# Kernel optimization log

Measured on AMD Instinct MI355X. Metric: run time of the kernel, lower is better.

The kernel has to match this reference:

```python
import jax, jax.numpy as jnp
import numpy as np

D = 128        # feature dim (hard-coded 128 split in source)
C = 16         # number of classes
N_S = 1600     # support set size (C * 100 shots)
Q = 32768      # number of query samples
HID = 128      # Class_Adap hidden width


def _class_centers(support_feat_inv, support_features, support_labels):
    # per-class mean of both support tensors (ComputeClassCenters)
    ones = jnp.ones((support_labels.shape[0],), support_feat_inv.dtype)
    counts = jax.ops.segment_sum(ones, support_labels, num_segments=C)
    counts = jnp.maximum(counts, 1.0)[:, None]                     # [C,1]
    mean_s = jax.ops.segment_sum(support_feat_inv, support_labels, num_segments=C) / counts   # [C,D]
    pre_s = jax.ops.segment_sum(support_features, support_labels, num_segments=C) / counts    # [C,D]
    return mean_s, pre_s


def setup_inputs() -> dict:
    key = jax.random.key(0)
    ks = jax.random.split(key, 6)
    return {
        "support_feat_inv": jax.random.normal(ks[0], (N_S, D), jnp.float32),
        "support_features": jax.random.normal(ks[1], (N_S, D), jnp.float32),
        "query_features": jax.random.normal(ks[2], (Q, D), jnp.float32),
        "W1": jax.random.normal(ks[3], (2 * D + 1, HID), jnp.float32) * 0.05,
        "b1": jnp.zeros((HID,), jnp.float32),
        "W2": jax.random.normal(ks[4], (HID, 1), jnp.float32) * 0.05,
        "b2": jnp.zeros((1,), jnp.float32),
        "support_labels": jax.random.randint(ks[5], (N_S,), 0, C),
        "query_labels": jax.random.randint(jax.random.fold_in(key, 7), (Q,), 0, C),
    }


def reference(support_feat_inv, support_features, query_features, W1, b1, W2, b2,
              support_labels, query_labels) -> jnp.ndarray:
    mean_s, pre_s = _class_centers(support_feat_inv, support_features, support_labels)
    q = query_features[:, None, :]                                  # [Q,1,D]
    gated = jax.nn.sigmoid(mean_s)[None, :, :] * q                  # [Q,C,D]
    q_full = jnp.broadcast_to(q, gated.shape)                       # [Q,C,D]
    inp = jnp.concatenate([q_full, gated], axis=-1)                 # [Q,C,2D]
    # AdaptiveAvgPool2d((None, D)) on [C,1,2D]: average adjacent pairs along last dim
    pooled = inp.reshape(Q, C, D, 2).mean(axis=-1)                  # [Q,C,D]
    # inner/outer product: sum(pre_support * query) per class
    outer = jnp.sum(pre_s[None, :, :] * q, axis=-1, keepdims=True)  # [Q,C,1]
    ext = jnp.concatenate([inp, outer], axis=-1)                    # [Q,C,2D+1]
    # Class_Adap tiny MLP -> per-class scalar weight
    h = jax.nn.relu(jnp.einsum('qce,eh->qch', ext, W1) + b1)        # [Q,C,HID]
    w = jax.nn.sigmoid(jnp.einsum('qch,ho->qco', h, W2) + b2)       # [Q,C,1]
    agg = jnp.sum(pooled * w, axis=1)                               # [Q,D]
    return agg + query_features                                     # residual (query_feature[0])
```

## Files before the change

### kernel.cpp

```cpp
#include <hip/hip_runtime.h>
#include <hip/hip_bf16.h>
#include <stdint.h>

#define DD 128
#define CC 16
#define NS 1600
#define QQ 32768
#define NBLK 64

typedef __attribute__((ext_vector_type(8))) short short8;
typedef __attribute__((ext_vector_type(4))) float f32x4;

__device__ inline short f2bf(float x) {
  union { float f; uint32_t u; } v; v.f = x;
  uint32_t r = (v.u + 0x7FFFu + ((v.u >> 16) & 1u)) >> 16;
  return (short)r;
}

__device__ inline uint32_t pk2bf(float lo, float hi) {
  __hip_bfloat162 h = __float22bfloat162_rn(make_float2(lo, hi));
  union { __hip_bfloat162 h2; uint32_t u; } v; v.h2 = h;
  return v.u;
}

__global__ __launch_bounds__(256) void centers_partial(
    const float* __restrict__ sfi, const float* __restrict__ sf,
    const int* __restrict__ labels, float* __restrict__ partA,
    float* __restrict__ partB, float* __restrict__ pcnt) {
  __shared__ float accA[2][CC][DD];
  __shared__ float accB[2][CC][DD];
  __shared__ float cnt[2][CC];
  const int t = threadIdx.x;
  const int d = t & 127, s = t >> 7;
  for (int i = t; i < 2 * CC * DD; i += 256) {
    ((float*)accA)[i] = 0.f;
    ((float*)accB)[i] = 0.f;
  }
  if (t < 2 * CC) ((float*)cnt)[t] = 0.f;
  __syncthreads();

  const int base = blockIdx.x * (NS / NBLK);
  for (int i = s; i < NS / NBLK; i += 2) {
    const int r = base + i;
    const int lbl = labels[r];
    accA[s][lbl][d] += sfi[(size_t)r * DD + d];
    accB[s][lbl][d] += sf[(size_t)r * DD + d];
    if (d == 0) cnt[s][lbl] += 1.f;
  }
  __syncthreads();

  float* pa = partA + (size_t)blockIdx.x * (CC * DD);
  float* pb = partB + (size_t)blockIdx.x * (CC * DD);
  for (int i = t; i < CC * DD; i += 256) {
    pa[i] = ((float*)accA)[i] + ((float*)accA)[CC * DD + i];
    pb[i] = ((float*)accB)[i] + ((float*)accB)[CC * DD + i];
  }
  if (t < CC) pcnt[blockIdx.x * CC + t] = cnt[0][t] + cnt[1][t];
}

__global__ __launch_bounds__(256) void build_wt_kernel(
    const float* __restrict__ W1, const float* __restrict__ partA,
    const float* __restrict__ partB, const float* __restrict__ pcnt,
    float* __restrict__ sg_out, short* __restrict__ WtTg) {
  __shared__ float sgc[DD], prc[DD];
  const int c = blockIdx.x, t = threadIdx.x;

  float cnt = 0.f;
  for (int b = 0; b < NBLK; ++b) cnt += pcnt[b * CC + c];
  cnt = fmaxf(cnt, 1.f);
  if (t < 128) {
    float a = 0.f;
    for (int b = 0; b < NBLK; ++b) a += partA[(size_t)b * (CC * DD) + c * DD + t];
    const float m = a / cnt;
    const float s = 1.f / (1.f + expf(-m));
    sgc[t] = s;
    sg_out[c * DD + t] = s;
  } else {
    const int d = t - 128;
    float a = 0.f;
    for (int b = 0; b < NBLK; ++b) a += partB[(size_t)b * (CC * DD) + c * DD + d];
    prc[d] = a / cnt;
  }
  __syncthreads();

  for (int it = 0; it < 8; ++it) {
    const int u = it * 256 + t;
    const int w_ = u >> 8;
    const int kb = (u >> 6) & 3;
    const int lane = u & 63;
    const int j = w_ * 16 + (lane & 15);
    const int e0 = kb * 32 + (lane >> 4) * 8;
    short8 r;
#pragma unroll
    for (int rr = 0; rr < 8; ++rr) {
      const int e = e0 + rr;
      float v = W1[e * DD + j] + sgc[e] * W1[(DD + e) * DD + j] +
                prc[e] * W1[2 * DD * DD + j];
      r[rr] = f2bf(v);
    }
    *(short8*)(WtTg + ((size_t)c * 2048 + u) * 8) = r;
  }
}

__global__ __launch_bounds__(512, 2) void main_kernel(
    const float* __restrict__ qf, const short* __restrict__ WtTg,
    const float* __restrict__ b1, const float* __restrict__ W2,
    const float* __restrict__ b2, float* __restrict__ w_ws) {
  __shared__ float p_part[8][CC][128];

  const int tid = threadIdx.x;
  const int lane = tid & 63;
  const int w = tid >> 6;
  const int l15 = lane & 15, l4 = lane >> 4;
  const int qbase = blockIdx.x * 128;

  short8 bq[8][4];
#pragma unroll
  for (int qn = 0; qn < 8; ++qn) {
    const float* qrow = qf + (size_t)(qbase + qn * 16 + l15) * DD;
#pragma unroll
    for (int kb = 0; kb < 4; ++kb) {
      const float* p0 = qrow + kb * 32 + l4 * 8;
      f32x4 f0 = *(const f32x4*)(p0);
      f32x4 f1 = *(const f32x4*)(p0 + 4);
      union { short8 s; uint32_t u[4]; } r;
      r.u[0] = pk2bf(f0[0], f0[1]);
      r.u[1] = pk2bf(f0[2], f0[3]);
      r.u[2] = pk2bf(f1[0], f1[1]);
      r.u[3] = pk2bf(f1[2], f1[3]);
      bq[qn][kb] = r.s;
    }
  }

  const f32x4 b1v = *(const f32x4*)(b1 + w * 16 + l4 * 4);
  const f32x4 w2v = *(const f32x4*)(W2 + w * 16 + l4 * 4);
  const float b2s = b2[0];

  const char* wbase = (const char*)WtTg + w * 4096 + lane * 16;

#define LOADW(dst, cls)                                                     \
  {                                                                         \
    _Pragma("unroll") for (int kb = 0; kb < 4; ++kb) dst[kb] =              \
        *(const short8*)(wbase + (size_t)(cls)*32768 + kb * 1024);          \
  }

#define COMPUTE(wf, cls)                                                    \
  {                                                                         \
    f32x4 acc[8];                                                           \
    _Pragma("unroll") for (int qn = 0; qn < 8; ++qn) acc[qn] = b1v;         \
    _Pragma("unroll") for (int kb = 0; kb < 4; ++kb)                        \
        _Pragma("unroll") for (int qn = 0; qn < 8; ++qn) acc[qn] =          \
            __builtin_amdgcn_mfma_f32_16x16x32_bf16(wf[kb], bq[qn][kb],     \
                                                    acc[qn], 0, 0, 0);      \
    _Pragma("unroll") for (int qn = 0; qn < 8; ++qn) {                      \
      float p = 0.f;                                                        \
      _Pragma("unroll") for (int i = 0; i < 4; ++i)                         \
          p += fmaxf(acc[qn][i], 0.f) * w2v[i];                             \
      p += __shfl_xor(p, 16);                                               \
      p += __shfl_xor(p, 32);                                               \
      if (l4 == 0) p_part[w][cls][qn * 16 + l15] = p;                       \
    }                                                                       \
  }

  short8 wfA[4], wfB[4];
  LOADW(wfA, 0);
  for (int c = 0; c < CC; c += 2) {
    LOADW(wfB, c + 1);
    COMPUTE(wfA, c);
    if (c + 2 < CC) LOADW(wfA, c + 2);
    COMPUTE(wfB, c + 1);
  }
#undef LOADW
#undef COMPUTE

  __syncthreads();

  {
    const int q = tid & 127;
    const int cg = tid >> 7;
    float pv[4];
#pragma unroll
    for (int k = 0; k < 4; ++k) {
      const int c = cg * 4 + k;
      float s = 0.f;
#pragma unroll
      for (int wv = 0; wv < 8; ++wv) s += p_part[wv][c][q];
      pv[k] = 1.f / (1.f + __expf(-(s + b2s)));
    }
    f32x4 o = {pv[0], pv[1], pv[2], pv[3]};
    *(f32x4*)(w_ws + ((size_t)(qbase + q)) * 16 + cg * 4) = o;
  }
}

__global__ __launch_bounds__(256) void agg_kernel(
    const float* __restrict__ qf, const float* __restrict__ sg,
    const float* __restrict__ w_ws, float* __restrict__ out) {
  const int t = threadIdx.x;
  const int s = t >> 5;
  const int ec = t & 31;
  const int e0 = ec * 4;
  const int qbase = blockIdx.x * 64;

  float4 sgv[16];
#pragma unroll
  for (int c = 0; c < 16; ++c) sgv[c] = *(const float4*)(sg + c * DD + e0);

  for (int qi = 0; qi < 8; ++qi) {
    const int q = qbase + qi * 8 + s;
    const float* wr = w_ws + (size_t)q * 16;
    float4 w0 = *(const float4*)(wr);
    float4 w1 = *(const float4*)(wr + 4);
    float4 w2 = *(const float4*)(wr + 8);
    float4 w3 = *(const float4*)(wr + 12);
    const float wc[16] = {w0.x, w0.y, w0.z, w0.w, w1.x, w1.y, w1.z, w1.w,
                          w2.x, w2.y, w2.z, w2.w, w3.x, w3.y, w3.z, w3.w};
    float Sv = 0.f;
#pragma unroll
    for (int c = 0; c < 16; ++c) Sv += wc[c];

    f32x4 sgw = {0.f, 0.f, 0.f, 0.f};
#pragma unroll
    for (int c = 0; c < 16; ++c) {
      sgw.x += wc[c] * sgv[c].x;
      sgw.y += wc[c] * sgv[c].y;
      sgw.z += wc[c] * sgv[c].z;
      sgw.w += wc[c] * sgv[c].w;
    }

    const float* qrow = qf + (size_t)q * DD;
    float4 qa = *(const float4*)(qrow + e0);
    float2 qd = *(const float2*)(qrow + 2 * ec);
    float2 qu = *(const float2*)(qrow + 64 + 2 * ec);

    float2 lo, hi;
    lo.x = 0.5f * (qa.x + qa.y) * Sv + qd.x;
    lo.y = 0.5f * (qa.z + qa.w) * Sv + qd.y;
    hi.x = 0.5f * (qa.x * sgw.x + qa.y * sgw.y) + qu.x;
    hi.y = 0.5f * (qa.z * sgw.z + qa.w * sgw.w) + qu.y;

    float* orow = out + (size_t)q * DD;
    *(float2*)(orow + 2 * ec) = lo;
    *(float2*)(orow + 64 + 2 * ec) = hi;
  }
}

extern "C" void kernel_launch(void* const* d_in, const int* in_sizes, int n_in,
                              void* d_out, int out_size, void* d_ws, size_t ws_size,
                              hipStream_t stream) {
  const float* sfi = (const float*)d_in[0];
  const float* sf  = (const float*)d_in[1];
  const float* qf  = (const float*)d_in[2];
  const float* W1  = (const float*)d_in[3];
  const float* b1  = (const float*)d_in[4];
  const float* W2  = (const float*)d_in[5];
  const float* b2  = (const float*)d_in[6];
  const int* slab  = (const int*)d_in[7];
  float* out = (float*)d_out;

  float* sg    = (float*)d_ws;
  float* w_ws  = sg + CC * DD;
  short* WtTg  = (short*)(w_ws + (size_t)QQ * CC);
  float* partA = (float*)(WtTg + CC * DD * DD);
  float* partB = partA + NBLK * CC * DD;
  float* pcnt  = partB + NBLK * CC * DD;

  centers_partial<<<NBLK, 256, 0, stream>>>(sfi, sf, slab, partA, partB, pcnt);
  build_wt_kernel<<<CC, 256, 0, stream>>>(W1, partA, partB, pcnt, sg, WtTg);
  main_kernel<<<QQ / 128, 512, 0, stream>>>(qf, WtTg, b1, W2, b2, w_ws);
  agg_kernel<<<QQ / 64, 256, 0, stream>>>(qf, sg, w_ws, out);
}
```

Before: 65.92 us.

## Pre-convert queries to bf16 in prep kernel and halve main kernel tile

Result: faster. 57.22 us (-13.2%).

```diff
diff --git a/kernel.cpp b/kernel.cpp
--- a/kernel.cpp
+++ b/kernel.cpp
@@ -9,6 +9,7 @@
 #define NBLK 64
 
 typedef __attribute__((ext_vector_type(8))) short short8;
+typedef __attribute__((ext_vector_type(4))) short short4v;
 typedef __attribute__((ext_vector_type(4))) float f32x4;
 
 __device__ inline short f2bf(float x) {
@@ -23,14 +24,30 @@
   return v.u;
 }
 
-__global__ __launch_bounds__(256) void centers_partial(
+__global__ __launch_bounds__(256) void prep_kernel(
     const float* __restrict__ sfi, const float* __restrict__ sf,
-    const int* __restrict__ labels, float* __restrict__ partA,
-    float* __restrict__ partB, float* __restrict__ pcnt) {
+    const int* __restrict__ labels, const float* __restrict__ qf,
+    float* __restrict__ partA, float* __restrict__ partB,
+    float* __restrict__ pcnt, short* __restrict__ qbf) {
+  const int t = threadIdx.x;
+
+  if (blockIdx.x >= NBLK) {
+    const size_t cb = (size_t)(blockIdx.x - NBLK) * (128 * DD);
+#pragma unroll
+    for (int i = 0; i < 16; ++i) {
+      const size_t off = cb + ((size_t)i * 256 + t) * 4;
+      f32x4 f = *(const f32x4*)(qf + off);
+      union { short4v s; uint32_t u[2]; } r;
+      r.u[0] = pk2bf(f[0], f[1]);
+      r.u[1] = pk2bf(f[2], f[3]);
+      *(short4v*)(qbf + off) = r.s;
+    }
+    return;
+  }
+
   __shared__ float accA[2][CC][DD];
   __shared__ float accB[2][CC][DD];
   __shared__ float cnt[2][CC];
-  const int t = threadIdx.x;
   const int d = t & 127, s = t >> 7;
   for (int i = t; i < 2 * CC * DD; i += 256) {
     ((float*)accA)[i] = 0.f;
@@ -102,34 +119,25 @@
   }
 }
 
-__global__ __launch_bounds__(512, 2) void main_kernel(
-    const float* __restrict__ qf, const short* __restrict__ WtTg,
+__global__ __launch_bounds__(512, 4) void main_kernel(
+    const short* __restrict__ qbf, const short* __restrict__ WtTg,
     const float* __restrict__ b1, const float* __restrict__ W2,
     const float* __restrict__ b2, float* __restrict__ w_ws) {
-  __shared__ float p_part[8][CC][128];
+  __shared__ float p_part[8][CC][64];
 
   const int tid = threadIdx.x;
   const int lane = tid & 63;
   const int w = tid >> 6;
   const int l15 = lane & 15, l4 = lane >> 4;
-  const int qbase = blockIdx.x * 128;
-
-  short8 bq[8][4];
-#pragma unroll
-  for (int qn = 0; qn < 8; ++qn) {
-    const float* qrow = qf + (size_t)(qbase + qn * 16 + l15) * DD;
-#pragma unroll
-    for (int kb = 0; kb < 4; ++kb) {
-      const float* p0 = qrow + kb * 32 + l4 * 8;
-      f32x4 f0 = *(const f32x4*)(p0);
-      f32x4 f1 = *(const f32x4*)(p0 + 4);
-      union { short8 s; uint32_t u[4]; } r;
-      r.u[0] = pk2bf(f0[0], f0[1]);
-      r.u[1] = pk2bf(f0[2], f0[3]);
-      r.u[2] = pk2bf(f1[0], f1[1]);
-      r.u[3] = pk2bf(f1[2], f1[3]);
-      bq[qn][kb] = r.s;
-    }
+  const int qbase = blockIdx.x * 64;
+
+  short8 bq[4][4];
+#pragma unroll
+  for (int qn = 0; qn < 4; ++qn) {
+    const short* qrow = qbf + (size_t)(qbase + qn * 16 + l15) * DD;
+#pragma unroll
+    for (int kb = 0; kb < 4; ++kb)
+      bq[qn][kb] = *(const short8*)(qrow + kb * 32 + l4 * 8);
   }
 
   const f32x4 b1v = *(const f32x4*)(b1 + w * 16 + l4 * 4);
@@ -146,19 +154,29 @@
 
 #define COMPUTE(wf, cls)                                                    \
   {                                                                         \
-    f32x4 acc[8];                                                           \
-    _Pragma("unroll") for (int qn = 0; qn < 8; ++qn) acc[qn] = b1v;         \
-    _Pragma("unroll") for (int kb = 0; kb < 4; ++kb)                        \
-        _Pragma("unroll") for (int qn = 0; qn < 8; ++qn) acc[qn] =          \
-            __builtin_amdgcn_mfma_f32_16x16x32_bf16(wf[kb], bq[qn][kb],     \
-                                                    acc[qn], 0, 0, 0);      \
-    _Pragma("unroll") for (int qn = 0; qn < 8; ++qn) {                      \
-      float p = 0.f;                                                        \
-      _Pragma("unroll") for (int i = 0; i < 4; ++i)                         \
-          p += fmaxf(acc[qn][i], 0.f) * w2v[i];                             \
-      p += __shfl_xor(p, 16);                                               \
-      p += __shfl_xor(p, 32);                                               \
-      if (l4 == 0) p_part[w][cls][qn * 16 + l15] = p;                       \
+    _Pragma("unroll") for (int qp = 0; qp < 2; ++qp) {                      \
+      f32x4 a0 = b1v, a1 = b1v;                                             \
+      _Pragma("unroll") for (int kb = 0; kb < 4; ++kb) {                    \
+        a0 = __builtin_amdgcn_mfma_f32_16x16x32_bf16(wf[kb],                \
+                                                     bq[2 * qp][kb], a0,    \
+                                                     0, 0, 0);              \
+        a1 = __builtin_amdgcn_mfma_f32_16x16x32_bf16(wf[kb],                \
+                                                     bq[2 * qp + 1][kb],    \
+                                                     a1, 0, 0, 0);          \
+      }                                                                     \
+      float p0 = 0.f, p1 = 0.f;                                             \
+      _Pragma("unroll") for (int i = 0; i < 4; ++i) {                       \
+        p0 += fmaxf(a0[i], 0.f) * w2v[i];                                   \
+        p1 += fmaxf(a1[i], 0.f) * w2v[i];                                   \
+      }                                                                     \
+      p0 += __shfl_xor(p0, 16);                                             \
+      p0 += __shfl_xor(p0, 32);                                             \
+      p1 += __shfl_xor(p1, 16);                                             \
+      p1 += __shfl_xor(p1, 32);                                             \
+      if (l4 == 0) {                                                        \
+        p_part[w][cls][(2 * qp) * 16 + l15] = p0;                           \
+        p_part[w][cls][(2 * qp + 1) * 16 + l15] = p1;                       \
+      }                                                                     \
     }                                                                       \
   }
 
@@ -176,19 +194,18 @@
   __syncthreads();
 
   {
-    const int q = tid & 127;
-    const int cg = tid >> 7;
-    float pv[4];
-#pragma unroll
-    for (int k = 0; k < 4; ++k) {
-      const int c = cg * 4 + k;
-      float s = 0.f;
-#pragma unroll
-      for (int wv = 0; wv < 8; ++wv) s += p_part[wv][c][q];
-      pv[k] = 1.f / (1.f + __expf(-(s + b2s)));
-    }
-    f32x4 o = {pv[0], pv[1], pv[2], pv[3]};
-    *(f32x4*)(w_ws + ((size_t)(qbase + q)) * 16 + cg * 4) = o;
+    const int q = tid & 63;
+    const int cg = tid >> 6;
+    float s0 = 0.f, s1 = 0.f;
+#pragma unroll
+    for (int wv = 0; wv < 8; ++wv) {
+      s0 += p_part[wv][cg * 2][q];
+      s1 += p_part[wv][cg * 2 + 1][q];
+    }
+    float2 o;
+    o.x = 1.f / (1.f + __expf(-(s0 + b2s)));
+    o.y = 1.f / (1.f + __expf(-(s1 + b2s)));
+    *(float2*)(w_ws + ((size_t)(qbase + q)) * 16 + cg * 2) = o;
   }
 }
 
@@ -263,9 +280,11 @@
   float* partA = (float*)(WtTg + CC * DD * DD);
   float* partB = partA + NBLK * CC * DD;
   float* pcnt  = partB + NBLK * CC * DD;
-
-  centers_partial<<<NBLK, 256, 0, stream>>>(sfi, sf, slab, partA, partB, pcnt);
+  short* qbf   = (short*)(pcnt + NBLK * CC);
+
+  prep_kernel<<<NBLK + QQ / 128, 256, 0, stream>>>(sfi, sf, slab, qf, partA,
+                                                   partB, pcnt, qbf);
   build_wt_kernel<<<CC, 256, 0, stream>>>(W1, partA, partB, pcnt, sg, WtTg);
-  main_kernel<<<QQ / 128, 512, 0, stream>>>(qf, WtTg, b1, W2, b2, w_ws);
+  main_kernel<<<QQ / 64, 512, 0, stream>>>(qbf, WtTg, b1, W2, b2, w_ws);
   agg_kernel<<<QQ / 64, 256, 0, stream>>>(qf, sg, w_ws, out);
 }
```

## Fuse aggregation into MLP kernel and halve queries per block

Applied to the files above, without the earlier changes.

Result: slower. 85.01 us (+28.9%).

```diff
diff --git a/kernel.cpp b/kernel.cpp
--- a/kernel.cpp
+++ b/kernel.cpp
@@ -102,21 +102,23 @@
   }
 }
 
-__global__ __launch_bounds__(512, 2) void main_kernel(
+__global__ __launch_bounds__(512, 4) void main_kernel(
     const float* __restrict__ qf, const short* __restrict__ WtTg,
     const float* __restrict__ b1, const float* __restrict__ W2,
-    const float* __restrict__ b2, float* __restrict__ w_ws) {
-  __shared__ float p_part[8][CC][128];
+    const float* __restrict__ b2, const float* __restrict__ sg,
+    float* __restrict__ out) {
+  __shared__ __align__(16) char p_lds[65536];
+  __shared__ float w_lds[64][17];
 
   const int tid = threadIdx.x;
   const int lane = tid & 63;
   const int w = tid >> 6;
   const int l15 = lane & 15, l4 = lane >> 4;
-  const int qbase = blockIdx.x * 128;
-
-  short8 bq[8][4];
-#pragma unroll
-  for (int qn = 0; qn < 8; ++qn) {
+  const int qbase = blockIdx.x * 64;
+
+  short8 bq[4][4];
+#pragma unroll
+  for (int qn = 0; qn < 4; ++qn) {
     const float* qrow = qf + (size_t)(qbase + qn * 16 + l15) * DD;
 #pragma unroll
     for (int kb = 0; kb < 4; ++kb) {
@@ -146,101 +148,98 @@
 
 #define COMPUTE(wf, cls)                                                    \
   {                                                                         \
-    f32x4 acc[8];                                                           \
-    _Pragma("unroll") for (int qn = 0; qn < 8; ++qn) acc[qn] = b1v;         \
-    _Pragma("unroll") for (int kb = 0; kb < 4; ++kb)                        \
-        _Pragma("unroll") for (int qn = 0; qn < 8; ++qn) acc[qn] =          \
-            __builtin_amdgcn_mfma_f32_16x16x32_bf16(wf[kb], bq[qn][kb],     \
-                                                    acc[qn], 0, 0, 0);      \
-    _Pragma("unroll") for (int qn = 0; qn < 8; ++qn) {                      \
-      float p = 0.f;                                                        \
-      _Pragma("unroll") for (int i = 0; i < 4; ++i)                         \
-          p += fmaxf(acc[qn][i], 0.f) * w2v[i];                             \
-      p += __shfl_xor(p, 16);                                               \
-      p += __shfl_xor(p, 32);                                               \
-      if (l4 == 0) p_part[w][cls][qn * 16 + l15] = p;                       \
+    f32x4 pv;                                                               \
+    _Pragma("unroll") for (int qp = 0; qp < 2; ++qp) {                      \
+      f32x4 a0 = b1v, a1 = b1v;                                             \
+      _Pragma("unroll") for (int kb = 0; kb < 4; ++kb) {                    \
+        a0 = __builtin_amdgcn_mfma_f32_16x16x32_bf16(wf[kb],                \
+                                                     bq[2 * qp][kb], a0,    \
+                                                     0, 0, 0);              \
+        a1 = __builtin_amdgcn_mfma_f32_16x16x32_bf16(wf[kb],                \
+                                                     bq[2 * qp + 1][kb],    \
+                                                     a1, 0, 0, 0);          \
+      }                                                                     \
+      float p0 = 0.f, p1 = 0.f;                                             \
+      _Pragma("unroll") for (int i = 0; i < 4; ++i) {                       \
+        p0 += fmaxf(a0[i], 0.f) * w2v[i];                                   \
+        p1 += fmaxf(a1[i], 0.f) * w2v[i];                                   \
+      }                                                                     \
+      pv[2 * qp] = p0;                                                      \
+      pv[2 * qp + 1] = p1;                                                  \
     }                                                                       \
+    *(f32x4*)(p_lds + (((cls)&7) * 8 + w) * 1024 + lane * 16) = pv;         \
+  }
+
+#define REDUCE(hf)                                                          \
+  {                                                                         \
+    __syncthreads();                                                        \
+    if (tid < 128) {                                                        \
+      const int c7 = tid >> 4, lr = tid & 15;                               \
+      f32x4 vacc = {0.f, 0.f, 0.f, 0.f};                                    \
+      _Pragma("unroll") for (int wv = 0; wv < 8; ++wv)                      \
+          _Pragma("unroll") for (int g = 0; g < 4; ++g) vacc +=             \
+          *(const f32x4*)(p_lds + (c7 * 8 + wv) * 1024 + (g * 16 + lr) * 16);\
+      _Pragma("unroll") for (int qn = 0; qn < 4; ++qn)                      \
+          w_lds[qn * 16 + lr][(hf)*8 + c7] =                                \
+              1.f / (1.f + __expf(-(vacc[qn] + b2s)));                      \
+    }                                                                       \
+    __syncthreads();                                                        \
   }
 
   short8 wfA[4], wfB[4];
   LOADW(wfA, 0);
-  for (int c = 0; c < CC; c += 2) {
-    LOADW(wfB, c + 1);
-    COMPUTE(wfA, c);
-    if (c + 2 < CC) LOADW(wfA, c + 2);
-    COMPUTE(wfB, c + 1);
+#pragma unroll
+  for (int cp = 0; cp < CC; cp += 2) {
+    LOADW(wfB, cp + 1);
+    COMPUTE(wfA, cp);
+    if (cp + 2 < CC) LOADW(wfA, cp + 2);
+    COMPUTE(wfB, cp + 1);
+    if (cp == 6) REDUCE(0);
+    if (cp == 14) REDUCE(1);
   }
 #undef LOADW
 #undef COMPUTE
-
-  __syncthreads();
+#undef REDUCE
 
   {
-    const int q = tid & 127;
-    const int cg = tid >> 7;
-    float pv[4];
-#pragma unroll
-    for (int k = 0; k < 4; ++k) {
-      const int c = cg * 4 + k;
-      float s = 0.f;
-#pragma unroll
-      for (int wv = 0; wv < 8; ++wv) s += p_part[wv][c][q];
-      pv[k] = 1.f / (1.f + __expf(-(s + b2s)));
+    const int s = tid >> 5;
+    const int ec = tid & 31;
+    const int e0 = ec * 4;
+
+    f32x4 sgv[16];
+#pragma unroll
+    for (int c = 0; c < 16; ++c) sgv[c] = *(const f32x4*)(sg + c * DD + e0);
+
+#pragma unroll
+    for (int qi = 0; qi < 4; ++qi) {
+      const int ql = qi * 16 + s;
+      const int q = qbase + ql;
+      float wc[16];
+      float Sv = 0.f;
+#pragma unroll
+      for (int c = 0; c < 16; ++c) {
+        wc[c] = w_lds[ql][c];
+        Sv += wc[c];
+      }
+      f32x4 sgw = {0.f, 0.f, 0.f, 0.f};
+#pragma unroll
+      for (int c = 0; c < 16; ++c) sgw += wc[c] * sgv[c];
+
+      const float* qrow = qf + (size_t)q * DD;
+      f32x4 qa = *(const f32x4*)(qrow + e0);
+      float2 qd = *(const float2*)(qrow + 2 * ec);
+      float2 qu = *(const float2*)(qrow + 64 + 2 * ec);
+
+      float2 lo, hi;
+      lo.x = 0.5f * (qa[0] + qa[1]) * Sv + qd.x;
+      lo.y = 0.5f * (qa[2] + qa[3]) * Sv + qd.y;
+      hi.x = 0.5f * (qa[0] * sgw[0] + qa[1] * sgw[1]) + qu.x;
+      hi.y = 0.5f * (qa[2] * sgw[2] + qa[3] * sgw[3]) + qu.y;
+
+      float* orow = out + (size_t)q * DD;
+      *(float2*)(orow + 2 * ec) = lo;
+      *(float2*)(orow + 64 + 2 * ec) = hi;
     }
-    f32x4 o = {pv[0], pv[1], pv[2], pv[3]};
-    *(f32x4*)(w_ws + ((size_t)(qbase + q)) * 16 + cg * 4) = o;
-  }
-}
-
-__global__ __launch_bounds__(256) void agg_kernel(
-    const float* __restrict__ qf, const float* __restrict__ sg,
-    const float* __restrict__ w_ws, float* __restrict__ out) {
-  const int t = threadIdx.x;
-  const int s = t >> 5;
-  const int ec = t & 31;
-  const int e0 = ec * 4;
-  const int qbase = blockIdx.x * 64;
-
-  float4 sgv[16];
-#pragma unroll
-  for (int c = 0; c < 16; ++c) sgv[c] = *(const float4*)(sg + c * DD + e0);
-
-  for (int qi = 0; qi < 8; ++qi) {
-    const int q = qbase + qi * 8 + s;
-    const float* wr = w_ws + (size_t)q * 16;
-    float4 w0 = *(const float4*)(wr);
-    float4 w1 = *(const float4*)(wr + 4);
-    float4 w2 = *(const float4*)(wr + 8);
-    float4 w3 = *(const float4*)(wr + 12);
-    const float wc[16] = {w0.x, w0.y, w0.z, w0.w, w1.x, w1.y, w1.z, w1.w,
-                          w2.x, w2.y, w2.z, w2.w, w3.x, w3.y, w3.z, w3.w};
-    float Sv = 0.f;
-#pragma unroll
-    for (int c = 0; c < 16; ++c) Sv += wc[c];
-
-    f32x4 sgw = {0.f, 0.f, 0.f, 0.f};
-#pragma unroll
-    for (int c = 0; c < 16; ++c) {
-      sgw.x += wc[c] * sgv[c].x;
-      sgw.y += wc[c] * sgv[c].y;
-      sgw.z += wc[c] * sgv[c].z;
-      sgw.w += wc[c] * sgv[c].w;
-    }
-
-    const float* qrow = qf + (size_t)q * DD;
-    float4 qa = *(const float4*)(qrow + e0);
-    float2 qd = *(const float2*)(qrow + 2 * ec);
-    float2 qu = *(const float2*)(qrow + 64 + 2 * ec);
-
-    float2 lo, hi;
-    lo.x = 0.5f * (qa.x + qa.y) * Sv + qd.x;
-    lo.y = 0.5f * (qa.z + qa.w) * Sv + qd.y;
-    hi.x = 0.5f * (qa.x * sgw.x + qa.y * sgw.y) + qu.x;
-    hi.y = 0.5f * (qa.z * sgw.z + qa.w * sgw.w) + qu.y;
-
-    float* orow = out + (size_t)q * DD;
-    *(float2*)(orow + 2 * ec) = lo;
-    *(float2*)(orow + 64 + 2 * ec) = hi;
   }
 }
 
@@ -258,14 +257,12 @@
   float* out = (float*)d_out;
 
   float* sg    = (float*)d_ws;
-  float* w_ws  = sg + CC * DD;
-  short* WtTg  = (short*)(w_ws + (size_t)QQ * CC);
+  short* WtTg  = (short*)(sg + CC * DD);
   float* partA = (float*)(WtTg + CC * DD * DD);
   float* partB = partA + NBLK * CC * DD;
   float* pcnt  = partB + NBLK * CC * DD;
 
   centers_partial<<<NBLK, 256, 0, stream>>>(sfi, sf, slab, partA, partB, pcnt);
   build_wt_kernel<<<CC, 256, 0, stream>>>(W1, partA, partB, pcnt, sg, WtTg);
-  main_kernel<<<QQ / 128, 512, 0, stream>>>(qf, WtTg, b1, W2, b2, w_ws);
-  agg_kernel<<<QQ / 64, 256, 0, stream>>>(qf, sg, w_ws, out);
-}
+  main_kernel<<<QQ / 64, 512, 0, stream>>>(qf, WtTg, b1, W2, b2, sg, out);
+}
```
